# Kernel optimization log

Measured on AMD Instinct MI355X. Metric: run time of the kernel, lower is better.

## Reference

```python
import jax, jax.numpy as jnp
import numpy as np

B, I, H = 8192, 1024, 1024

def setup_inputs() -> dict:
    key = jax.random.key(0)
    ks = jax.random.split(key, 5)
    # xavier-uniform-ish scale for weights
    sW = float(np.sqrt(6.0 / (I + H)))
    sU = float(np.sqrt(6.0 / (H + H)))
    return {
        "x": jax.random.normal(ks[0], (B, I), jnp.float32),
        "h": jax.random.normal(ks[1], (B, H), jnp.float32),
        "c": jax.random.normal(ks[2], (B, H), jnp.float32),
        # gate order along leading axis: 0=i, 1=f, 2=o, 3=c_hat
        "W": jax.random.uniform(ks[3], (4, H, I), jnp.float32, -sW, sW),
        "bW": jnp.zeros((4, H), jnp.float32),
        "U": jax.random.uniform(ks[4], (4, H, H), jnp.float32, -sU, sU),
        "bU": jnp.zeros((4, H), jnp.float32),
    }

def reference(x, h, c, W, bW, U, bU):
    # two batched GEMMs covering all 8 original Linear layers
    gx = jnp.einsum('bi,ghi->gbh', x, W) + bW[:, None, :]   # [4,B,H]
    gh = jnp.einsum('bk,ghk->gbh', h, U) + bU[:, None, :]   # [4,B,H]
    g = gx + gh
    i = jax.nn.sigmoid(g[0])
    f = jax.nn.sigmoid(g[1])
    o = jax.nn.sigmoid(g[2])
    c_hat = jnp.tanh(g[3])
    c_new = f * c + i * c_hat
    h_new = o * jnp.tanh(c_new)
    return (h_new, (h_new, c_new))
```

## Files before the change

### kernel.cpp

```cpp
#include <hip/hip_runtime.h>
#include <hip/hip_bf16.h>

typedef __hip_bfloat16 bf16;
typedef __attribute__((ext_vector_type(8))) short short8;
typedef __attribute__((ext_vector_type(4))) float floatx4;

#define B_DIM 8192
#define H_DIM 1024
#define KSUM 2048
#define BM 256
#define BN 256
#define BK 64
#define KT 32
#define NSLOT 10
#define SLOT_ELEMS 8192
#define CEX_STRIDE 68

union BS { bf16 b; short s; };
__device__ __forceinline__ short cvt1(float f) {
  BS u; u.b = __float2bfloat16(f); return u.s;
}
__device__ __forceinline__ short8 cvt8(float4 lo, float4 hi) {
  short8 r;
  r[0] = cvt1(lo.x); r[1] = cvt1(lo.y); r[2] = cvt1(lo.z); r[3] = cvt1(lo.w);
  r[4] = cvt1(hi.x); r[5] = cvt1(hi.y); r[6] = cvt1(hi.z); r[7] = cvt1(hi.w);
  return r;
}

__device__ __forceinline__ void async_ld16(const bf16* g, bf16* lds) {
  __builtin_amdgcn_global_load_lds(
      (const __attribute__((address_space(1))) unsigned int*)g,
      (__attribute__((address_space(3))) unsigned int*)lds,
      16, 0, 0);
}

__global__ __launch_bounds__(256) void cvt_pack(
    const float* __restrict__ x, const float* __restrict__ h,
    const float* __restrict__ W, const float* __restrict__ U,
    bf16* __restrict__ Ac, bf16* __restrict__ Bc) {
  const int blk = blockIdx.x;
  if (blk < 8192) {
    const int idx = blk * 256 + threadIdx.x;
    const long row = idx >> 8;
    const int k0 = (idx & 255) << 3;
    const float* src = (k0 < 1024) ? (x + row * 1024 + k0)
                                   : (h + row * 1024 + (k0 - 1024));
    const float4 lo = *(const float4*)src;
    const float4 hi = *(const float4*)(src + 4);
    *(short8*)(Ac + row * KSUM + k0) = cvt8(lo, hi);
  } else {
    const int idx = (blk - 8192) * 256 + threadIdx.x;
    const long r = idx >> 8;
    const int k0 = (idx & 255) << 3;
    const int g = (int)(r & 3);
    const long hh = r >> 2;
    const long base = (long)g * (H_DIM * H_DIM) + hh * H_DIM;
    const float* src = (k0 < 1024) ? (W + base + k0) : (U + base + (k0 - 1024));
    const float4 lo = *(const float4*)src;
    const float4 hi = *(const float4*)(src + 4);
    *(short8*)(Bc + r * KSUM + k0) = cvt8(lo, hi);
  }
}

__device__ __forceinline__ float sigmoidf_(float v) {
  return 1.0f / (1.0f + __expf(-v));
}
__device__ __forceinline__ float tanhf_(float v) {
  return 1.0f - 2.0f / (__expf(2.0f * v) + 1.0f);
}
__device__ __forceinline__ float getc(const float4& v, int t) {
  return t == 0 ? v.x : t == 1 ? v.y : t == 2 ? v.z : v.w;
}

__global__ __launch_bounds__(512, 2) void gemm_lstm(
    const bf16* __restrict__ Ac, const bf16* __restrict__ Bc,
    const float* __restrict__ cprev_g, const float* __restrict__ bW,
    const float* __restrict__ bU, float* __restrict__ out) {
  extern __shared__ __align__(16) char smem[];
  bf16* const ring = (bf16*)smem;
  float* const cex = (float*)smem;

  const int tid  = threadIdx.x;
  const int lane = tid & 63;
  const int wv   = tid >> 6;
  const int wm_idx = wv >> 2;
  const int wn_idx = wv & 3;

  const int blk  = blockIdx.x;
  const int xcd  = blk & 7;
  const int slot = blk >> 3;
  const int mt   = slot & 31;
  const int nt   = (xcd << 1) | (slot >> 5);
  const long m0 = (long)mt * BM;
  const long n0 = (long)nt * BN;

  const int lrow   = lane >> 3;
  const int lchunk = lane & 7;
  const int schunk = lchunk ^ lrow;
  const bf16* const aRow0 = Ac + (m0 + wv * 8 + lrow) * (long)KSUM + schunk * 8;
  const bf16* const bRow0 = Bc + (n0 + wv * 8 + lrow) * (long)KSUM + schunk * 8;

  const int col16 = lane & 15;
  const int quad  = lane >> 4;
  const int x7    = col16 & 7;
  const int bRowOff = (wn_idx & 1) << 6;

  floatx4 acc[8][4];
#pragma unroll
  for (int i = 0; i < 8; ++i)
#pragma unroll
    for (int jq = 0; jq < 4; ++jq) acc[i][jq] = (floatx4){0.f, 0.f, 0.f, 0.f};

#define STAGE_HALF(h_)                                                        \
  {                                                                           \
    const int c_ = (h_) & 3;                                                  \
    const long off_ = ((long)((c_ >> 1) * 128)) * KSUM + (long)(((h_) >> 2) * BK); \
    const bf16* s_ = ((c_ & 1) ? bRow0 : aRow0) + off_;                       \
    bf16* d_ = ring + ((h_) % NSLOT) * SLOT_ELEMS + wv * 512;                 \
    async_ld16(s_, d_);                                                       \
    async_ld16(s_ + 64L * KSUM, d_ + 4096);                                   \
  }

#define READ_AF(rh_)                                                          \
  _Pragma("unroll") for (int fi = 0; fi < 4; ++fi)                            \
    _Pragma("unroll") for (int s = 0; s < 2; ++s)                             \
      af_[fi][s] = *(const short8*)&rA[((rh_) * 64 + fi * 16 + col16) * 64 +  \
                                       ((((s << 2) + quad) ^ x7) << 3)];

#define READ_BF(nh_)                                                          \
  _Pragma("unroll") for (int fj = 0; fj < 2; ++fj)                            \
    _Pragma("unroll") for (int s = 0; s < 2; ++s)                             \
      bf_[fj][s] = *(const short8*)&rB[(bRowOff + (nh_) * 32 + fj * 16 + col16) * 64 + \
                                       ((((s << 2) + quad) ^ x7) << 3)];

#define STAGE_P(p_)                                                           \
  { const int h_ = 4 * j + (p_) + 6; if (h_ < 4 * KT) STAGE_HALF(h_); }

#define SYNC_MID()                                                            \
  __builtin_amdgcn_s_barrier();                                               \
  asm volatile("s_waitcnt lgkmcnt(0)" ::: "memory");                          \
  __builtin_amdgcn_sched_barrier(0);

#define MFMA_Q(rh_, nh_)                                                      \
  __builtin_amdgcn_s_setprio(1);                                              \
  _Pragma("unroll") for (int fi = 0; fi < 4; ++fi)                            \
    _Pragma("unroll") for (int fj = 0; fj < 2; ++fj)                          \
      _Pragma("unroll") for (int s = 0; s < 2; ++s)                           \
        acc[(rh_) * 4 + fi][(nh_) * 2 + fj] =                                 \
            __builtin_amdgcn_mfma_f32_16x16x32_bf16(                          \
                af_[fi][s], bf_[fj][s], acc[(rh_) * 4 + fi][(nh_) * 2 + fj],  \
                0, 0, 0);                                                     \
  __builtin_amdgcn_s_setprio(0);

#pragma unroll
  for (int h = 0; h < 6; ++h) STAGE_HALF(h);
  asm volatile("s_waitcnt vmcnt(4)" ::: "memory");
  __builtin_amdgcn_s_barrier();

#pragma unroll 1
  for (int j = 0; j < KT; ++j) {
    const bf16* const rA =
        ring + ((4 * j + 2 * wm_idx) % NSLOT) * SLOT_ELEMS;
    const bf16* const rB =
        ring + ((4 * j + 1 + ((wn_idx >> 1) << 1)) % NSLOT) * SLOT_ELEMS;
    short8 af_[4][2], bf_[2][2];

    READ_AF(0) READ_BF(0) STAGE_P(0) SYNC_MID() MFMA_Q(0, 0)
    __builtin_amdgcn_s_barrier();
    READ_BF(1) STAGE_P(1) SYNC_MID() MFMA_Q(0, 1)
    __builtin_amdgcn_s_barrier();
    READ_AF(1) READ_BF(0) STAGE_P(2) SYNC_MID() MFMA_Q(1, 0)
    __builtin_amdgcn_s_barrier();
    READ_BF(1) STAGE_P(3) SYNC_MID() MFMA_Q(1, 1)
    if (j < KT - 2) asm volatile("s_waitcnt vmcnt(4)" ::: "memory");
    else            asm volatile("s_waitcnt vmcnt(0)" ::: "memory");
    __builtin_amdgcn_s_barrier();
  }

  const int rquad = (lane >> 4) << 2;
  const int row16 = lane & 15;
  const int tq    = lane >> 4;
  const long hglob = ((n0 + (long)(wn_idx << 6)) >> 2) + tq * 4;

  float4 bsum[4];
#pragma unroll
  for (int g = 0; g < 4; ++g) {
    const float4 a = *(const float4*)(bW + g * H_DIM + hglob);
    const float4 b = *(const float4*)(bU + g * H_DIM + hglob);
    bsum[g] = (float4){a.x + b.x, a.y + b.y, a.z + b.z, a.w + b.w};
  }

  float* wx = cex + wv * (16 * CEX_STRIDE);
  const long BH = (long)B_DIM * H_DIM;

#pragma unroll
  for (int ig = 0; ig < 8; ++ig) {
#pragma unroll
    for (int jj = 0; jj < 4; ++jj)
#pragma unroll
      for (int r = 0; r < 4; ++r)
        wx[(rquad + r) * CEX_STRIDE + jj * 16 + col16] = acc[ig][jj][r];

    float4 g4[4];
#pragma unroll
    for (int t = 0; t < 4; ++t)
      g4[t] = *(const float4*)&wx[row16 * CEX_STRIDE + (tq * 4 + t) * 4];

    const long mrow = m0 + (long)wm_idx * 128 + ig * 16 + row16;
    const float4 cp4 = *(const float4*)(cprev_g + mrow * H_DIM + hglob);

    float hn[4], cn[4];
#pragma unroll
    for (int t = 0; t < 4; ++t) {
      const float gi = g4[t].x + getc(bsum[0], t);
      const float gf = g4[t].y + getc(bsum[1], t);
      const float go = g4[t].z + getc(bsum[2], t);
      const float gg = g4[t].w + getc(bsum[3], t);
      const float I = sigmoidf_(gi);
      const float F = sigmoidf_(gf);
      const float O = sigmoidf_(go);
      const float G = tanhf_(gg);
      const float cv = F * getc(cp4, t) + I * G;
      hn[t] = O * tanhf_(cv);
      cn[t] = cv;
    }
    const float4 hn4 = {hn[0], hn[1], hn[2], hn[3]};
    const float4 cn4 = {cn[0], cn[1], cn[2], cn[3]};
    const long ob = mrow * H_DIM + hglob;
    *(float4*)(out + ob)          = hn4;
    *(float4*)(out + BH + ob)     = hn4;
    *(float4*)(out + 2 * BH + ob) = cn4;
  }
}

extern "C" void kernel_launch(void* const* d_in, const int* in_sizes, int n_in,
                              void* d_out, int out_size, void* d_ws, size_t ws_size,
                              hipStream_t stream) {
  const float* x  = (const float*)d_in[0];
  const float* h  = (const float*)d_in[1];
  const float* c  = (const float*)d_in[2];
  const float* W  = (const float*)d_in[3];
  const float* bW = (const float*)d_in[4];
  const float* U  = (const float*)d_in[5];
  const float* bU = (const float*)d_in[6];
  float* out = (float*)d_out;

  bf16* Ac = (bf16*)d_ws;
  bf16* Bc = (bf16*)((char*)d_ws + (size_t)33554432);

  static bool attr_done = false;
  if (!attr_done) {
    hipFuncSetAttribute(reinterpret_cast<const void*>(gemm_lstm),
                        hipFuncAttributeMaxDynamicSharedMemorySize, 163840);
    attr_done = true;
  }

  cvt_pack<<<12288, 256, 0, stream>>>(x, h, W, U, Ac, Bc);
  gemm_lstm<<<512, 512, 163840, stream>>>(Ac, Bc, c, bW, bU, out);
}
```

Baseline: 348.9 us.

## Restructure K-loop into two phases with full B fragments reused across both row halves

```diff
diff --git a/kernel.cpp b/kernel.cpp
--- a/kernel.cpp
+++ b/kernel.cpp
@@ -121,35 +121,26 @@
     async_ld16(s_ + 64L * KSUM, d_ + 4096);                                   \
   }
 
-#define READ_AF(rh_)                                                          \
-  _Pragma("unroll") for (int fi = 0; fi < 4; ++fi)                            \
-    _Pragma("unroll") for (int s = 0; s < 2; ++s)                             \
-      af_[fi][s] = *(const short8*)&rA[((rh_) * 64 + fi * 16 + col16) * 64 +  \
-                                       ((((s << 2) + quad) ^ x7) << 3)];
-
-#define READ_BF(nh_)                                                          \
-  _Pragma("unroll") for (int fj = 0; fj < 2; ++fj)                            \
-    _Pragma("unroll") for (int s = 0; s < 2; ++s)                             \
-      bf_[fj][s] = *(const short8*)&rB[(bRowOff + (nh_) * 32 + fj * 16 + col16) * 64 + \
-                                       ((((s << 2) + quad) ^ x7) << 3)];
-
 #define STAGE_P(p_)                                                           \
   { const int h_ = 4 * j + (p_) + 6; if (h_ < 4 * KT) STAGE_HALF(h_); }
 
-#define SYNC_MID()                                                            \
-  __builtin_amdgcn_s_barrier();                                               \
-  asm volatile("s_waitcnt lgkmcnt(0)" ::: "memory");                          \
-  __builtin_amdgcn_sched_barrier(0);
-
-#define MFMA_Q(rh_, nh_)                                                      \
+#define READ_AF_S(rh_, s_)                                                    \
+  _Pragma("unroll") for (int fi = 0; fi < 4; ++fi)                            \
+    af_[fi][s_] = *(const short8*)&rA[((rh_) * 64 + fi * 16 + col16) * 64 +   \
+                                      (((((s_) << 2) + quad) ^ x7) << 3)];
+
+#define READ_BF_S(s_)                                                         \
+  _Pragma("unroll") for (int fj = 0; fj < 4; ++fj)                            \
+    bf_[fj][s_] = *(const short8*)&rB[(bRowOff + fj * 16 + col16) * 64 +      \
+                                      (((((s_) << 2) + quad) ^ x7) << 3)];
+
+#define MFMA_HALF(rh_)                                                        \
   __builtin_amdgcn_s_setprio(1);                                              \
-  _Pragma("unroll") for (int fi = 0; fi < 4; ++fi)                            \
-    _Pragma("unroll") for (int fj = 0; fj < 2; ++fj)                          \
-      _Pragma("unroll") for (int s = 0; s < 2; ++s)                           \
-        acc[(rh_) * 4 + fi][(nh_) * 2 + fj] =                                 \
-            __builtin_amdgcn_mfma_f32_16x16x32_bf16(                          \
-                af_[fi][s], bf_[fj][s], acc[(rh_) * 4 + fi][(nh_) * 2 + fj],  \
-                0, 0, 0);                                                     \
+  _Pragma("unroll") for (int s = 0; s < 2; ++s)                               \
+    _Pragma("unroll") for (int fi = 0; fi < 4; ++fi)                          \
+      _Pragma("unroll") for (int fj = 0; fj < 4; ++fj)                        \
+        acc[(rh_) * 4 + fi][fj] = __builtin_amdgcn_mfma_f32_16x16x32_bf16(    \
+            af_[fi][s], bf_[fj][s], acc[(rh_) * 4 + fi][fj], 0, 0, 0);        \
   __builtin_amdgcn_s_setprio(0);
 
 #pragma unroll
@@ -163,15 +154,26 @@
         ring + ((4 * j + 2 * wm_idx) % NSLOT) * SLOT_ELEMS;
     const bf16* const rB =
         ring + ((4 * j + 1 + ((wn_idx >> 1) << 1)) % NSLOT) * SLOT_ELEMS;
-    short8 af_[4][2], bf_[2][2];
-
-    READ_AF(0) READ_BF(0) STAGE_P(0) SYNC_MID() MFMA_Q(0, 0)
-    __builtin_amdgcn_s_barrier();
-    READ_BF(1) STAGE_P(1) SYNC_MID() MFMA_Q(0, 1)
-    __builtin_amdgcn_s_barrier();
-    READ_AF(1) READ_BF(0) STAGE_P(2) SYNC_MID() MFMA_Q(1, 0)
-    __builtin_amdgcn_s_barrier();
-    READ_BF(1) STAGE_P(3) SYNC_MID() MFMA_Q(1, 1)
+    short8 af_[4][2], bf_[4][2];
+
+    READ_AF_S(0, 0) READ_BF_S(0)
+    __builtin_amdgcn_sched_barrier(0);
+    READ_AF_S(0, 1) READ_BF_S(1)
+    __builtin_amdgcn_sched_barrier(0);
+    STAGE_P(0) STAGE_P(1)
+    __builtin_amdgcn_sched_barrier(0);
+    __builtin_amdgcn_s_barrier();
+    MFMA_HALF(0)
+    __builtin_amdgcn_s_barrier();
+
+    READ_AF_S(1, 0)
+    __builtin_amdgcn_sched_barrier(0);
+    READ_AF_S(1, 1)
+    __builtin_amdgcn_sched_barrier(0);
+    STAGE_P(2) STAGE_P(3)
+    __builtin_amdgcn_sched_barrier(0);
+    __builtin_amdgcn_s_barrier();
+    MFMA_HALF(1)
     if (j < KT - 2) asm volatile("s_waitcnt vmcnt(4)" ::: "memory");
     else            asm volatile("s_waitcnt vmcnt(0)" ::: "memory");
     __builtin_amdgcn_s_barrier();
```

Measured after the change: 337.4 us. 3.3% less time.
